# Kernel tuning notes

Hardware: AMD Instinct MI355X
Metric: run time of the kernel (lower is better)

## Reference

```python
import jax, jax.numpy as jnp
import numpy as np

VOCAB = 30
D_MODEL = 512
D_K = 64
D_V = 64
N_HEAD = 8
D_FF = 2048
N_LAYERS = 4
LN_EPS = 1e-5


def _make_pe(max_len, d_model):
    pos = np.arange(max_len, dtype=np.float32)[:, None]
    div = np.exp(np.arange(0, d_model, 2, dtype=np.float32) * (-np.log(10000.0) / d_model))
    pe = np.zeros((max_len, d_model), dtype=np.float32)
    pe[:, 0::2] = np.sin(pos * div)
    pe[:, 1::2] = np.cos(pos * div)
    return jnp.asarray(pe)


def setup_inputs() -> dict:
    key = jax.random.key(0)
    ks = jax.random.split(key, 16)
    B, S = 4, 2048
    s = 0.02
    inp = {
        "input_ids": jax.random.randint(ks[0], (B, S), 0, VOCAB, dtype=jnp.int64),
        "attn_mask": jax.random.randint(ks[1], (B, S), 0, 2, dtype=jnp.int64),
        "tok_embed": jax.random.normal(ks[2], (VOCAB, D_MODEL), jnp.float32) * s,
        "pe": _make_pe(S, D_MODEL),
        "Wq": jax.random.normal(ks[3], (N_LAYERS, D_MODEL, N_HEAD * D_K), jnp.float32) * s,
        "Wk": jax.random.normal(ks[4], (N_LAYERS, D_MODEL, N_HEAD * D_K), jnp.float32) * s,
        "Wv": jax.random.normal(ks[5], (N_LAYERS, D_MODEL, N_HEAD * D_V), jnp.float32) * s,
        "Wo": jax.random.normal(ks[6], (N_LAYERS, N_HEAD * D_V, D_MODEL), jnp.float32) * s,
        "ln1_g": jnp.ones((N_LAYERS, D_MODEL), jnp.float32),
        "ln1_b": jnp.zeros((N_LAYERS, D_MODEL), jnp.float32),
        "W1": jax.random.normal(ks[7], (N_LAYERS, D_MODEL, D_FF), jnp.float32) * s,
        "W2": jax.random.normal(ks[8], (N_LAYERS, D_FF, D_MODEL), jnp.float32) * s,
        "ln2_g": jnp.ones((N_LAYERS, D_MODEL), jnp.float32),
        "ln2_b": jnp.zeros((N_LAYERS, D_MODEL), jnp.float32),
    }
    return inp


def _layernorm(x, g, b):
    mu = jnp.mean(x, axis=-1, keepdims=True)
    var = jnp.mean(jnp.square(x - mu), axis=-1, keepdims=True)
    return (x - mu) * jax.lax.rsqrt(var + LN_EPS) * g + b


def reference(input_ids, attn_mask, tok_embed, pe, Wq, Wk, Wv, Wo, ln1_g, ln1_b, W1, W2, ln2_g, ln2_b):
    B, S = input_ids.shape
    x = tok_embed[input_ids] + pe[:S][None]  # [B,S,D]
    # pad mask: key positions where attn_mask==0, broadcast over heads & queries
    pad = (attn_mask == 0)[:, None, None, :]  # [B,1,1,S]
    scale = 1.0 / np.sqrt(D_K)
    for l in range(N_LAYERS):
        # multi-head self-attention
        q = (x @ Wq[l]).reshape(B, S, N_HEAD, D_K)
        k = (x @ Wk[l]).reshape(B, S, N_HEAD, D_K)
        v = (x @ Wv[l]).reshape(B, S, N_HEAD, D_V)
        scores = jnp.einsum('bqhd,bkhd->bhqk', q, k) * scale
        scores = jnp.where(pad, -1e9, scores)
        attn = jax.nn.softmax(scores, axis=-1)
        ctx = jnp.einsum('bhqk,bkhd->bqhd', attn, v).reshape(B, S, N_HEAD * D_V)
        x = _layernorm(ctx @ Wo[l] + x, ln1_g[l], ln1_b[l])
        # position-wise FFN
        h = jax.nn.relu(x @ W1[l])
        x = _layernorm(h @ W2[l] + x, ln2_g[l], ln2_b[l])
    return x
```

## Files before the change

### kernel.cpp

```cpp
#include <hip/hip_runtime.h>
#include <stdint.h>

#define S_LEN 2048
#define B_SZ 4
#define DM 512
#define NTOK (B_SZ * S_LEN)

typedef unsigned short u16;
typedef unsigned int u32;
typedef unsigned long long u64;
typedef __attribute__((ext_vector_type(8))) short short8;
typedef __attribute__((ext_vector_type(4))) float f32x4;

typedef const __attribute__((address_space(1))) u32 gq_t;
typedef __attribute__((address_space(3))) u32 lq_t;

__device__ __forceinline__ u16 f2bf(float f) {
  union { float f; u32 u; } v; v.f = f;
  return (u16)((v.u + 0x7FFFu + ((v.u >> 16) & 1u)) >> 16);
}

__device__ __forceinline__ float bf2f(u32 hi16_at_lo) {
  union { u32 u; float f; } v; v.u = hi16_at_lo;
  return v.f;
}

__device__ __forceinline__ float fexp2(float x) {
#if __has_builtin(__builtin_amdgcn_exp2f)
  return __builtin_amdgcn_exp2f(x);
#else
  return exp2f(x);
#endif
}

__device__ __forceinline__ short8 mk8(u64 a, u64 b) {
  union { u64 q[2]; short8 s; } u;
  u.q[0] = a; u.q[1] = b;
  return u.s;
}

__device__ __forceinline__ void swap32(u32& x, u32& y) {
  asm("v_permlane32_swap_b32 %0, %1" : "+v"(x), "+v"(y));
}
__device__ __forceinline__ void swap16(u32& x, u32& y, int lane) {
#if __has_builtin(__builtin_amdgcn_permlane16_swap)
  asm("v_permlane16_swap_b32 %0, %1" : "+v"(x), "+v"(y));
#else
  u32 tx = __builtin_amdgcn_ds_swizzle(x, 0x401F);
  u32 ty = __builtin_amdgcn_ds_swizzle(y, 0x401F);
  bool up = (lane & 16) != 0;
  u32 nx = up ? ty : x;
  u32 ny = up ? y : tx;
  x = nx; y = ny;
#endif
}

__global__ void embed_kernel(const int* __restrict__ ids, const float* __restrict__ te,
                             const float* __restrict__ pe, float* __restrict__ x,
                             u16* __restrict__ xb) {
  int gid = blockIdx.x * 256 + threadIdx.x;
  int tok = gid >> 7, c4 = (gid & 127) << 2;
  int s = tok & (S_LEN - 1);
  int id = ids[tok];
  const float4 a = *(const float4*)(te + (long)id * DM + c4);
  const float4 p = *(const float4*)(pe + (long)s * DM + c4);
  float4 o; o.x = a.x + p.x; o.y = a.y + p.y; o.z = a.z + p.z; o.w = a.w + p.w;
  *(float4*)(x + (long)tok * DM + c4) = o;
  uint2 pk;
  pk.x = (u32)f2bf(o.x) | ((u32)f2bf(o.y) << 16);
  pk.y = (u32)f2bf(o.z) | ((u32)f2bf(o.w) << 16);
  *(uint2*)(xb + (long)tok * DM + c4) = pk;
}

__global__ void wconv_kernel(const float* __restrict__ src, u16* __restrict__ dst,
                             int K, int N, int dstLayerStride, int noff, int total) {
  int gid = blockIdx.x * 256 + threadIdx.x;
  if (gid >= total) return;
  int k = gid % K;
  int n = (gid / K) % N;
  int l = gid / (K * N);
  dst[(long)l * dstLayerStride + (long)(noff + n) * K + k] =
      f2bf(src[(long)l * K * N + (long)k * N + n]);
}

template <int BM, int BN, bool OUT_BF16, bool RELU, bool VSPLIT>
__global__ __launch_bounds__(BM * 2) void gemm_kernel(const u16* __restrict__ A,
                                                      const u16* __restrict__ BT,
                                                      void* __restrict__ Cout,
                                                      u16* __restrict__ vt,
                                                      int M, int N, int K) {
  constexpr int NI = BN / 32;
  constexpr int NW = BM / 32;
  constexpr int BRW = BN / NW;
  __shared__ __align__(16) u16 a_t[2][BM * 64];
  __shared__ __align__(16) u16 b_t[2][BN * 64];
  const int tid = threadIdx.x;
  const int w = tid >> 6, lane = tid & 63;
  const int wr = w >> 1, wc = w & 1;
  const int g = lane >> 4, lr = lane & 15;
  const int l8 = lane >> 3, lch = lane & 7;
  const int gc = lch ^ l8;
  const int nwg = gridDim.x * gridDim.y;
  const int bid = blockIdx.x + gridDim.x * blockIdx.y;
  const int cpx = nwg >> 3;
  const int swz = (bid & 7) * cpx + (bid >> 3);
  const int bx = swz % gridDim.x, by = swz / gridDim.x;
  const long m0 = (long)by * BM, n0 = (long)bx * BN;
  f32x4 acc[4][NI] = {};
  const int nk = K >> 6;

  auto stage = [&](int nb, int k0) {
#pragma unroll
    for (int i = 0; i < 4; ++i) {
      int row = w * 32 + i * 8 + l8;
      __builtin_amdgcn_global_load_lds((gq_t*)(A + (m0 + row) * K + k0 + gc * 8),
                                       (lq_t*)&a_t[nb][(w * 4 + i) * 512], 16, 0, 0);
    }
#pragma unroll
    for (int i = 0; i < BRW / 8; ++i) {
      int row = w * BRW + i * 8 + l8;
      __builtin_amdgcn_global_load_lds((gq_t*)(BT + (n0 + row) * K + k0 + gc * 8),
                                       (lq_t*)&b_t[nb][(w * (BRW / 8) + i) * 512], 16, 0, 0);
    }
  };

  stage(0, 0);
  __syncthreads();
  for (int kt = 0; kt < nk; ++kt) {
    const int cur = kt & 1;
    if (kt + 1 < nk) stage(cur ^ 1, (kt + 1) << 6);
#pragma unroll
    for (int ks = 0; ks < 2; ++ks) {
      short8 af[4], bfr[NI];
#pragma unroll
      for (int mi = 0; mi < 4; ++mi) {
        int row = wr * 64 + mi * 16 + lr;
        int byte = row * 128 + (((ks * 4 + g) ^ (row & 7)) << 4);
        af[mi] = *(const short8*)((const char*)a_t[cur] + byte);
      }
#pragma unroll
      for (int ni = 0; ni < NI; ++ni) {
        int row = wc * (BN / 2) + ni * 16 + lr;
        int byte = row * 128 + (((ks * 4 + g) ^ (row & 7)) << 4);
        bfr[ni] = *(const short8*)((const char*)b_t[cur] + byte);
      }
#pragma unroll
      for (int mi = 0; mi < 4; ++mi)
#pragma unroll
        for (int ni = 0; ni < NI; ++ni)
          acc[mi][ni] = __builtin_amdgcn_mfma_f32_16x16x32_bf16(af[mi], bfr[ni], acc[mi][ni], 0, 0, 0);
    }
    __syncthreads();
  }

  if constexpr (VSPLIT) {
    if (n0 >= 1024) {
#pragma unroll
      for (int mi = 0; mi < 4; ++mi)
#pragma unroll
        for (int ni = 0; ni < NI; ++ni) {
          int vc = (int)(n0 - 1024) + wc * (BN / 2) + ni * 16 + lr;
          int hh = vc >> 6, d = vc & 63;
          long tok0 = m0 + wr * 64 + mi * 16 + g * 4;
          int bb = (int)(tok0 >> 11), s0 = (int)(tok0 & 2047);
          uint2 pk;
          pk.x = (u32)f2bf(acc[mi][ni][0]) | ((u32)f2bf(acc[mi][ni][1]) << 16);
          pk.y = (u32)f2bf(acc[mi][ni][2]) | ((u32)f2bf(acc[mi][ni][3]) << 16);
          *(uint2*)(vt + (((long)bb * 8 + hh) * 64 + d) * 2048 + s0) = pk;
        }
      return;
    }
  }
#pragma unroll
  for (int mi = 0; mi < 4; ++mi)
#pragma unroll
    for (int ni = 0; ni < NI; ++ni)
#pragma unroll
      for (int j = 0; j < 4; ++j) {
        long grow = m0 + wr * 64 + mi * 16 + g * 4 + j;
        long gcol = n0 + wc * (BN / 2) + ni * 16 + lr;
        float v = acc[mi][ni][j];
        if (RELU) v = fmaxf(v, 0.f);
        if (OUT_BF16) ((u16*)Cout)[grow * N + gcol] = f2bf(v);
        else ((float*)Cout)[grow * N + gcol] = v;
      }
}

__global__ __launch_bounds__(512) void attn_kernel(const u16* __restrict__ qkv,
                                                   const u16* __restrict__ vt,
                                                   const int* __restrict__ mask,
                                                   u16* __restrict__ ctx) {
  __shared__ __align__(16) u16 k_t[2][64 * 64];
  __shared__ __align__(16) u16 v_t[2][80 * 64];
  __shared__ __align__(16) u16 q_t[128 * 64];
  __shared__ __align__(16) float mvals[2][64];
  __shared__ __align__(16) float l_lds[128];
  const int tid = threadIdx.x;
  const int w = tid >> 6, lane = tid & 63;
  const int g = lane >> 4, lr = lane & 15;
  const int l8 = lane >> 3, lch = lane & 7;
  const int gc = lch ^ l8;
  const int b = blockIdx.z, h = blockIdx.y, q0 = blockIdx.x * 128;
  const long base = (long)b * S_LEN * 1536;
  const int qcol = h * 64, kcol = 512 + h * 64;
  const u16* vhead = vt + (((long)b * 8 + h) * 64) * 2048;
  const float SC = 0.18033688011112042f;

  auto stageKV = [&](int nb, int kb) {
    {
      int row = w * 8 + l8;
      __builtin_amdgcn_global_load_lds((gq_t*)(qkv + base + (long)(kb + row) * 1536 + kcol + gc * 8),
                                       (lq_t*)&k_t[nb][w * 512], 16, 0, 0);
    }
    {
      int row = w * 8 + l8;
      __builtin_amdgcn_global_load_lds((gq_t*)(vhead + (long)row * 2048 + kb + gc * 8),
                                       (lq_t*)&v_t[nb][w * 512], 16, 0, 0);
    }
    if (tid < 64) mvals[nb][tid] = (mask[b * S_LEN + kb + tid] == 0) ? -1e9f : 0.f;
  };

  {
    int r16 = tid >> 5;
    u32 val = (r16 == 0) ? 0x3F803F80u : 0u;
    *(u32*)((char*)v_t[0] + 64 * 128 + tid * 4) = val;
    *(u32*)((char*)v_t[1] + 64 * 128 + tid * 4) = val;
  }
#pragma unroll
  for (int i = 0; i < 2; ++i) {
    int e = i * 512 + tid;
    int row = e >> 3, ch = e & 7;
    uint4 v = *(const uint4*)(qkv + base + (long)(q0 + row) * 1536 + qcol + ch * 8);
    *(uint4*)((char*)q_t + row * 128 + ((ch ^ (row & 7)) << 4)) = v;
  }
  stageKV(0, 0);
  __syncthreads();
  short8 qf[2];
#pragma unroll
  for (int ks = 0; ks < 2; ++ks) {
    int row = w * 16 + lr;
    qf[ks] = *(const short8*)((const char*)q_t + row * 128 + (((ks * 4 + g) ^ (row & 7)) << 4));
  }

  f32x4 o[5] = {};

  for (int kt = 0; kt < S_LEN / 64; ++kt) {
    const int cur = kt & 1;
    if (kt + 1 < S_LEN / 64) stageKV(cur ^ 1, (kt + 1) * 64);

    f32x4 s[4] = {};
#pragma unroll
    for (int ks = 0; ks < 2; ++ks) {
#pragma unroll
      for (int ni = 0; ni < 4; ++ni) {
        int row = ni * 16 + lr;
        short8 kf = *(const short8*)((const char*)k_t[cur] + row * 128 + (((ks * 4 + g) ^ (row & 7)) << 4));
        s[ni] = __builtin_amdgcn_mfma_f32_16x16x32_bf16(kf, qf[ks], s[ni], 0, 0, 0);
      }
    }
    float p[4][4];
#pragma unroll
    for (int ni = 0; ni < 4; ++ni) {
      const float4 mv = *(const float4*)&mvals[cur][ni * 16 + 4 * g];
      const float mva[4] = {mv.x, mv.y, mv.z, mv.w};
#pragma unroll
      for (int r = 0; r < 4; ++r)
        p[ni][r] = fexp2(fmaf(s[ni][r], SC, mva[r]));
    }
    u32 wv[4][2];
#pragma unroll
    for (int ni = 0; ni < 4; ++ni)
#pragma unroll
      for (int pp = 0; pp < 2; ++pp)
        asm("v_cvt_pk_bf16_f32 %0, %1, %2"
            : "=v"(wv[ni][pp]) : "v"(p[ni][2 * pp]), "v"(p[ni][2 * pp + 1]));

    u32 x0 = wv[0][0], x1 = wv[0][1], y0 = wv[1][0], y1 = wv[1][1];
    swap32(x0, y0); swap32(x1, y1);
    swap16(x0, y0, lane); swap16(x1, y1, lane);
    short8 pa0 = mk8((u64)x0 | ((u64)x1 << 32), (u64)y0 | ((u64)y1 << 32));
    u32 x2 = wv[2][0], x3 = wv[2][1], y2 = wv[3][0], y3 = wv[3][1];
    swap32(x2, y2); swap32(x3, y3);
    swap16(x2, y2, lane); swap16(x3, y3, lane);
    short8 pa1 = mk8((u64)x2 | ((u64)x3 << 32), (u64)y2 | ((u64)y3 << 32));

#pragma unroll
    for (int ks2 = 0; ks2 < 2; ++ks2) {
      short8 pa = ks2 ? pa1 : pa0;
#pragma unroll
      for (int nd = 0; nd < 5; ++nd) {
        int vrow = nd * 16 + lr;
        short8 vf = *(const short8*)((const char*)v_t[cur] + vrow * 128 + (((ks2 * 4 + g) ^ (vrow & 7)) << 4));
        o[nd] = __builtin_amdgcn_mfma_f32_16x16x32_bf16(pa, vf, o[nd], 0, 0, 0);
      }
    }
    if (kt + 1 < S_LEN / 64) __syncthreads();
  }
  if (lr == 0) {
#pragma unroll
    for (int r = 0; r < 4; ++r) l_lds[w * 16 + 4 * g + r] = o[4][r];
  }
  const float4 lv = *(const float4*)&l_lds[w * 16 + 4 * g];
  const float la[4] = {lv.x, lv.y, lv.z, lv.w};
  float inv[4];
#pragma unroll
  for (int r = 0; r < 4; ++r) inv[r] = 1.f / la[r];
#pragma unroll
  for (int nd = 0; nd < 4; ++nd)
#pragma unroll
    for (int r = 0; r < 4; ++r) {
      int tok = q0 + w * 16 + 4 * g + r;
      int col = h * 64 + nd * 16 + lr;
      ctx[((long)b * S_LEN + tok) * 512 + col] = f2bf(o[nd][r] * inv[r]);
    }
}

template <bool YBF16>
__global__ __launch_bounds__(256) void ln_kernel(const void* __restrict__ yv_,
                                                 const float* __restrict__ res,
                                                 const float* __restrict__ gam,
                                                 const float* __restrict__ bet,
                                                 float* __restrict__ out,
                                                 u16* __restrict__ ob) {
  const int row = blockIdx.x, t = threadIdx.x;
  const long o0 = (long)row * DM;
  float y0, y1;
  if constexpr (YBF16) {
    u32 wbits = *(const u32*)((const u16*)yv_ + o0 + 2 * t);
    y0 = bf2f(wbits << 16);
    y1 = bf2f(wbits & 0xFFFF0000u);
  } else {
    const float2 yv = *(const float2*)((const float*)yv_ + o0 + 2 * t);
    y0 = yv.x; y1 = yv.y;
  }
  const float2 rv = *(const float2*)&res[o0 + 2 * t];
  float a0 = y0 + rv.x;
  float a1 = y1 + rv.y;
  float s1 = a0 + a1, s2 = a0 * a0 + a1 * a1;
#pragma unroll
  for (int m = 32; m >= 1; m >>= 1) {
    s1 += __shfl_xor(s1, m);
    s2 += __shfl_xor(s2, m);
  }
  __shared__ float w1[4], w2[4];
  if ((t & 63) == 0) { w1[t >> 6] = s1; w2[t >> 6] = s2; }
  __syncthreads();
  s1 = w1[0] + w1[1] + w1[2] + w1[3];
  s2 = w2[0] + w2[1] + w2[2] + w2[3];
  const float mu = s1 * (1.f / DM);
  const float rstd = rsqrtf(s2 * (1.f / DM) - mu * mu + 1e-5f);
  const float2 gv = *(const float2*)&gam[2 * t];
  const float2 bv = *(const float2*)&bet[2 * t];
  float r0 = (a0 - mu) * rstd * gv.x + bv.x;
  float r1 = (a1 - mu) * rstd * gv.y + bv.y;
  float2 ov; ov.x = r0; ov.y = r1;
  *(float2*)&out[o0 + 2 * t] = ov;
  if (ob) {
    u32 pk = (u32)f2bf(r0) | ((u32)f2bf(r1) << 16);
    *(u32*)&ob[o0 + 2 * t] = pk;
  }
}

extern "C" void kernel_launch(void* const* d_in, const int* in_sizes, int n_in,
                              void* d_out, int out_size, void* d_ws, size_t ws_size,
                              hipStream_t stream) {
  const int*   ids  = (const int*)d_in[0];
  const int*   amsk = (const int*)d_in[1];
  const float* te   = (const float*)d_in[2];
  const float* pe   = (const float*)d_in[3];
  const float* Wq   = (const float*)d_in[4];
  const float* Wk   = (const float*)d_in[5];
  const float* Wv   = (const float*)d_in[6];
  const float* Wo   = (const float*)d_in[7];
  const float* ln1g = (const float*)d_in[8];
  const float* ln1b = (const float*)d_in[9];
  const float* W1   = (const float*)d_in[10];
  const float* W2   = (const float*)d_in[11];
  const float* ln2g = (const float*)d_in[12];
  const float* ln2b = (const float*)d_in[13];
  float* out = (float*)d_out;

  char* p = (char*)d_ws;
  float* x   = (float*)p; p += (long)NTOK * DM * 4;
  u16* qkv   = (u16*)p;   p += (long)NTOK * 1536 * 2;
  u16* ctx   = (u16*)p;   p += (long)NTOK * DM * 2;
  u16* tmp   = (u16*)p;   p += (long)NTOK * DM * 4;
  u16* hb    = (u16*)p;   p += (long)NTOK * 2048 * 2;
  u16* WqkvT = (u16*)p;   p += (long)4 * 1536 * 512 * 2;
  u16* WoT   = (u16*)p;   p += (long)4 * 512 * 512 * 2;
  u16* W1T   = (u16*)p;   p += (long)4 * 2048 * 512 * 2;
  u16* W2T   = (u16*)p;   p += (long)4 * 512 * 2048 * 2;
  if ((size_t)(p - (char*)d_ws) > ws_size) return;
  u16* vt = hb;

  {
    int tq = 4 * 512 * 512;
    wconv_kernel<<<(tq + 255) / 256, 256, 0, stream>>>(Wq, WqkvT, 512, 512, 1536 * 512, 0, tq);
    wconv_kernel<<<(tq + 255) / 256, 256, 0, stream>>>(Wk, WqkvT, 512, 512, 1536 * 512, 512, tq);
    wconv_kernel<<<(tq + 255) / 256, 256, 0, stream>>>(Wv, WqkvT, 512, 512, 1536 * 512, 1024, tq);
    wconv_kernel<<<(tq + 255) / 256, 256, 0, stream>>>(Wo, WoT, 512, 512, 512 * 512, 0, tq);
    int t1 = 4 * 512 * 2048;
    wconv_kernel<<<(t1 + 255) / 256, 256, 0, stream>>>(W1, W1T, 512, 2048, 2048 * 512, 0, t1);
    wconv_kernel<<<(t1 + 255) / 256, 256, 0, stream>>>(W2, W2T, 2048, 512, 512 * 2048, 0, t1);
  }
  embed_kernel<<<NTOK * 128 / 256, 256, 0, stream>>>(ids, te, pe, x, ctx);

  for (int l = 0; l < 4; ++l) {
    gemm_kernel<256, 64, true, false, true><<<dim3(1536 / 64, NTOK / 256), 512, 0, stream>>>(
        ctx, WqkvT + (long)l * 1536 * 512, qkv, vt, NTOK, 1536, 512);
    attn_kernel<<<dim3(S_LEN / 128, 8, B_SZ), 512, 0, stream>>>(qkv, vt, amsk, ctx);
    gemm_kernel<128, 64, true, false, false><<<dim3(512 / 64, NTOK / 128), 256, 0, stream>>>(
        ctx, WoT + (long)l * 512 * 512, tmp, nullptr, NTOK, 512, 512);
    ln_kernel<true><<<NTOK, 256, 0, stream>>>(tmp, x, ln1g + l * 512, ln1b + l * 512, x, ctx);
    gemm_kernel<256, 64, true, true, false><<<dim3(2048 / 64, NTOK / 256), 512, 0, stream>>>(
        ctx, W1T + (long)l * 2048 * 512, hb, nullptr, NTOK, 2048, 512);
    gemm_kernel<128, 64, true, false, false><<<dim3(512 / 64, NTOK / 128), 256, 0, stream>>>(
        hb, W2T + (long)l * 512 * 2048, tmp, nullptr, NTOK, 512, 2048);
    ln_kernel<true><<<NTOK, 256, 0, stream>>>(tmp, x, ln2g + l * 512, ln2b + l * 512,
                                              (l == 3) ? out : x, (l == 3) ? (u16*)nullptr : ctx);
  }
}
```

Measured before the change: 698.8 us.

## Prefetch GEMM tiles two stages ahead and vectorize stores via swapped MFMA operands

The GEMM main loop now keeps two K-tiles in flight. It uses explicit vmcnt waits and raw barriers instead of __syncthreads. It loads all LDS fragments before issuing the next prefetch into the buffer just consumed, so global loads overlap the MFMA work. A SWAPC mode swaps the MFMA A/B operands so each lane holds four consecutive output columns, which allows packed 8-byte bf16 stores instead of scalar 2-byte stores. The six weight-conversion launches are also merged into one kernel to cut launch overhead. The hand-tuned waitcnt values depend on the per-thread load count per stage, which makes the code fragile if the tile shapes change.

```diff
diff --git a/kernel.cpp b/kernel.cpp
--- a/kernel.cpp
+++ b/kernel.cpp
@@ -72,18 +72,33 @@
   *(uint2*)(xb + (long)tok * DM + c4) = pk;
 }
 
-__global__ void wconv_kernel(const float* __restrict__ src, u16* __restrict__ dst,
-                             int K, int N, int dstLayerStride, int noff, int total) {
-  int gid = blockIdx.x * 256 + threadIdx.x;
-  if (gid >= total) return;
-  int k = gid % K;
-  int n = (gid / K) % N;
-  int l = gid / (K * N);
-  dst[(long)l * dstLayerStride + (long)(noff + n) * K + k] =
-      f2bf(src[(long)l * K * N + (long)k * N + n]);
-}
-
-template <int BM, int BN, bool OUT_BF16, bool RELU, bool VSPLIT>
+__global__ void wconv_all(const float* __restrict__ Wq, const float* __restrict__ Wk,
+                          const float* __restrict__ Wv, const float* __restrict__ Wo,
+                          const float* __restrict__ W1, const float* __restrict__ W2,
+                          u16* __restrict__ WqkvT, u16* __restrict__ WoT,
+                          u16* __restrict__ W1T, u16* __restrict__ W2T) {
+  long gid = (long)blockIdx.x * 256 + threadIdx.x;
+  const long SQ = 4L * 512 * 512;
+  const long SF = 4L * 512 * 2048;
+  const float* src; u16* dst; int K, N, ls, noff; long g2;
+  if (gid < 3 * SQ) {
+    int which = (int)(gid / SQ); g2 = gid % SQ;
+    src = which == 0 ? Wq : which == 1 ? Wk : Wv;
+    dst = WqkvT; K = 512; N = 512; ls = 1536 * 512; noff = 512 * which;
+  } else if (gid < 4 * SQ) {
+    g2 = gid - 3 * SQ; src = Wo; dst = WoT; K = 512; N = 512; ls = 512 * 512; noff = 0;
+  } else if (gid < 4 * SQ + SF) {
+    g2 = gid - 4 * SQ; src = W1; dst = W1T; K = 512; N = 2048; ls = 2048 * 512; noff = 0;
+  } else {
+    g2 = gid - 4 * SQ - SF; src = W2; dst = W2T; K = 2048; N = 512; ls = 512 * 2048; noff = 0;
+  }
+  int k = (int)(g2 % K);
+  int n = (int)((g2 / K) % N);
+  int l = (int)(g2 / ((long)K * N));
+  dst[(long)l * ls + (long)(noff + n) * K + k] = f2bf(src[(long)l * K * N + (long)k * N + n]);
+}
+
+template <int BM, int BN, bool RELU, bool VSPLIT, bool SWAPC>
 __global__ __launch_bounds__(BM * 2) void gemm_kernel(const u16* __restrict__ A,
                                                       const u16* __restrict__ BT,
                                                       void* __restrict__ Cout,
@@ -92,6 +107,7 @@
   constexpr int NI = BN / 32;
   constexpr int NW = BM / 32;
   constexpr int BRW = BN / NW;
+  constexpr int LOADS = 4 + BRW / 8;
   __shared__ __align__(16) u16 a_t[2][BM * 64];
   __shared__ __align__(16) u16 b_t[2][BN * 64];
   const int tid = threadIdx.x;
@@ -109,7 +125,8 @@
   f32x4 acc[4][NI] = {};
   const int nk = K >> 6;
 
-  auto stage = [&](int nb, int k0) {
+  auto stage = [&](int nb, int kt) {
+    const int k0 = kt << 6;
 #pragma unroll
     for (int i = 0; i < 4; ++i) {
       int row = w * 32 + i * 8 + l8;
@@ -125,32 +142,48 @@
   };
 
   stage(0, 0);
-  __syncthreads();
+  stage(1, 1);
   for (int kt = 0; kt < nk; ++kt) {
     const int cur = kt & 1;
-    if (kt + 1 < nk) stage(cur ^ 1, (kt + 1) << 6);
+    if (kt + 1 < nk) {
+      if constexpr (LOADS == 6) asm volatile("s_waitcnt vmcnt(6)" ::: "memory");
+      else                      asm volatile("s_waitcnt vmcnt(5)" ::: "memory");
+    } else {
+      asm volatile("s_waitcnt vmcnt(0)" ::: "memory");
+    }
+    __builtin_amdgcn_s_barrier();
+    __builtin_amdgcn_sched_barrier(0);
+    short8 af[2][4], bfr[2][NI];
 #pragma unroll
     for (int ks = 0; ks < 2; ++ks) {
-      short8 af[4], bfr[NI];
 #pragma unroll
       for (int mi = 0; mi < 4; ++mi) {
         int row = wr * 64 + mi * 16 + lr;
         int byte = row * 128 + (((ks * 4 + g) ^ (row & 7)) << 4);
-        af[mi] = *(const short8*)((const char*)a_t[cur] + byte);
+        af[ks][mi] = *(const short8*)((const char*)a_t[cur] + byte);
       }
 #pragma unroll
       for (int ni = 0; ni < NI; ++ni) {
         int row = wc * (BN / 2) + ni * 16 + lr;
         int byte = row * 128 + (((ks * 4 + g) ^ (row & 7)) << 4);
-        bfr[ni] = *(const short8*)((const char*)b_t[cur] + byte);
+        bfr[ks][ni] = *(const short8*)((const char*)b_t[cur] + byte);
       }
+    }
+    asm volatile("s_waitcnt lgkmcnt(0)" ::: "memory");
+    __builtin_amdgcn_s_barrier();
+    __builtin_amdgcn_sched_barrier(0);
+    if (kt + 2 < nk) stage(cur, kt + 2);
+#pragma unroll
+    for (int ks = 0; ks < 2; ++ks)
 #pragma unroll
       for (int mi = 0; mi < 4; ++mi)
 #pragma unroll
-        for (int ni = 0; ni < NI; ++ni)
-          acc[mi][ni] = __builtin_amdgcn_mfma_f32_16x16x32_bf16(af[mi], bfr[ni], acc[mi][ni], 0, 0, 0);
-    }
-    __syncthreads();
+        for (int ni = 0; ni < NI; ++ni) {
+          if constexpr (SWAPC)
+            acc[mi][ni] = __builtin_amdgcn_mfma_f32_16x16x32_bf16(bfr[ks][ni], af[ks][mi], acc[mi][ni], 0, 0, 0);
+          else
+            acc[mi][ni] = __builtin_amdgcn_mfma_f32_16x16x32_bf16(af[ks][mi], bfr[ks][ni], acc[mi][ni], 0, 0, 0);
+        }
   }
 
   if constexpr (VSPLIT) {
@@ -171,19 +204,36 @@
       return;
     }
   }
-#pragma unroll
-  for (int mi = 0; mi < 4; ++mi)
-#pragma unroll
-    for (int ni = 0; ni < NI; ++ni)
-#pragma unroll
-      for (int j = 0; j < 4; ++j) {
-        long grow = m0 + wr * 64 + mi * 16 + g * 4 + j;
-        long gcol = n0 + wc * (BN / 2) + ni * 16 + lr;
-        float v = acc[mi][ni][j];
-        if (RELU) v = fmaxf(v, 0.f);
-        if (OUT_BF16) ((u16*)Cout)[grow * N + gcol] = f2bf(v);
-        else ((float*)Cout)[grow * N + gcol] = v;
+  if constexpr (SWAPC) {
+#pragma unroll
+    for (int mi = 0; mi < 4; ++mi)
+#pragma unroll
+      for (int ni = 0; ni < NI; ++ni) {
+        long grow = m0 + wr * 64 + mi * 16 + lr;
+        long gcb = n0 + wc * (BN / 2) + ni * 16 + 4 * g;
+        float v0 = acc[mi][ni][0], v1 = acc[mi][ni][1], v2 = acc[mi][ni][2], v3 = acc[mi][ni][3];
+        if (RELU) {
+          v0 = fmaxf(v0, 0.f); v1 = fmaxf(v1, 0.f); v2 = fmaxf(v2, 0.f); v3 = fmaxf(v3, 0.f);
+        }
+        uint2 pk;
+        pk.x = (u32)f2bf(v0) | ((u32)f2bf(v1) << 16);
+        pk.y = (u32)f2bf(v2) | ((u32)f2bf(v3) << 16);
+        *(uint2*)((u16*)Cout + grow * N + gcb) = pk;
       }
+  } else {
+#pragma unroll
+    for (int mi = 0; mi < 4; ++mi)
+#pragma unroll
+      for (int ni = 0; ni < NI; ++ni)
+#pragma unroll
+        for (int j = 0; j < 4; ++j) {
+          long grow = m0 + wr * 64 + mi * 16 + g * 4 + j;
+          long gcol = n0 + wc * (BN / 2) + ni * 16 + lr;
+          float v = acc[mi][ni][j];
+          if (RELU) v = fmaxf(v, 0.f);
+          ((u16*)Cout)[grow * N + gcol] = f2bf(v);
+        }
+  }
 }
 
 __global__ __launch_bounds__(512) void attn_kernel(const u16* __restrict__ qkv,
@@ -394,27 +444,22 @@
   u16* vt = hb;
 
   {
-    int tq = 4 * 512 * 512;
-    wconv_kernel<<<(tq + 255) / 256, 256, 0, stream>>>(Wq, WqkvT, 512, 512, 1536 * 512, 0, tq);
-    wconv_kernel<<<(tq + 255) / 256, 256, 0, stream>>>(Wk, WqkvT, 512, 512, 1536 * 512, 512, tq);
-    wconv_kernel<<<(tq + 255) / 256, 256, 0, stream>>>(Wv, WqkvT, 512, 512, 1536 * 512, 1024, tq);
-    wconv_kernel<<<(tq + 255) / 256, 256, 0, stream>>>(Wo, WoT, 512, 512, 512 * 512, 0, tq);
-    int t1 = 4 * 512 * 2048;
-    wconv_kernel<<<(t1 + 255) / 256, 256, 0, stream>>>(W1, W1T, 512, 2048, 2048 * 512, 0, t1);
-    wconv_kernel<<<(t1 + 255) / 256, 256, 0, stream>>>(W2, W2T, 2048, 512, 512 * 2048, 0, t1);
+    long total = 4L * 512 * 512 * 4 + 2L * 4 * 512 * 2048;
+    wconv_all<<<(int)((total + 255) / 256), 256, 0, stream>>>(
+        Wq, Wk, Wv, Wo, W1, W2, WqkvT, WoT, W1T, W2T);
   }
   embed_kernel<<<NTOK * 128 / 256, 256, 0, stream>>>(ids, te, pe, x, ctx);
 
   for (int l = 0; l < 4; ++l) {
-    gemm_kernel<256, 64, true, false, true><<<dim3(1536 / 64, NTOK / 256), 512, 0, stream>>>(
+    gemm_kernel<256, 64, false, true, false><<<dim3(1536 / 64, NTOK / 256), 512, 0, stream>>>(
         ctx, WqkvT + (long)l * 1536 * 512, qkv, vt, NTOK, 1536, 512);
     attn_kernel<<<dim3(S_LEN / 128, 8, B_SZ), 512, 0, stream>>>(qkv, vt, amsk, ctx);
-    gemm_kernel<128, 64, true, false, false><<<dim3(512 / 64, NTOK / 128), 256, 0, stream>>>(
+    gemm_kernel<128, 64, false, false, true><<<dim3(512 / 64, NTOK / 128), 256, 0, stream>>>(
         ctx, WoT + (long)l * 512 * 512, tmp, nullptr, NTOK, 512, 512);
     ln_kernel<true><<<NTOK, 256, 0, stream>>>(tmp, x, ln1g + l * 512, ln1b + l * 512, x, ctx);
-    gemm_kernel<256, 64, true, true, false><<<dim3(2048 / 64, NTOK / 256), 512, 0, stream>>>(
+    gemm_kernel<256, 64, true, false, true><<<dim3(2048 / 64, NTOK / 256), 512, 0, stream>>>(
         ctx, W1T + (long)l * 2048 * 512, hb, nullptr, NTOK, 2048, 512);
-    gemm_kernel<128, 64, true, false, false><<<dim3(512 / 64, NTOK / 128), 256, 0, stream>>>(
+    gemm_kernel<128, 64, false, false, true><<<dim3(512 / 64, NTOK / 128), 256, 0, stream>>>(
         hb, W2T + (long)l * 512 * 2048, tmp, nullptr, NTOK, 512, 2048);
     ln_kernel<true><<<NTOK, 256, 0, stream>>>(tmp, x, ln2g + l * 512, ln2b + l * 512,
                                               (l == 3) ? out : x, (l == 3) ? (u16*)nullptr : ctx);
```

New measurement: 662.2 us. 5.2% less time.
